# Kernel optimization log

Hardware: AMD Instinct MI355X
Metric: run time of the kernel (lower is better)

Reference implementation:

```python
import jax, jax.numpy as jnp
import numpy as np

B, S, D = 4, 2048, 1024
H = 16
HD = D // H  # 64

def setup_inputs() -> dict:
    key = jax.random.key(0)
    ks = jax.random.split(key, 4)
    scale = 0.02
    return {
        "hidden_states": jax.random.normal(ks[0], (B, S, D), dtype=jnp.float32),
        "attention_mask": jnp.zeros((B, 1, 1, S), dtype=jnp.float32),
        "Wq": jax.random.normal(ks[1], (D, D), dtype=jnp.float32) * scale,
        "bq": jnp.zeros((D,), dtype=jnp.float32),
        "Wk": jax.random.normal(ks[2], (D, D), dtype=jnp.float32) * scale,
        "bk": jnp.zeros((D,), dtype=jnp.float32),
        "Wv": jax.random.normal(ks[3], (D, D), dtype=jnp.float32) * scale,
        "bv": jnp.zeros((D,), dtype=jnp.float32),
    }

def reference(hidden_states, attention_mask, Wq, bq, Wk, bk, Wv, bv):
    b, s, d = hidden_states.shape
    def proj(W, bias):
        # Linear then split heads: [b, s, d] -> [b, H, s, HD]
        y = hidden_states @ W.T + bias
        return y.reshape(b, s, H, HD).transpose(0, 2, 1, 3)
    Q = proj(Wq, bq)
    K = proj(Wk, bk)
    V = proj(Wv, bv)
    scores = jnp.einsum('bhqd,bhkd->bhqk', Q, K) / jnp.sqrt(jnp.float32(HD))
    scores = scores + attention_mask  # additive mask, broadcast [b,1,1,s]
    probs = jax.nn.softmax(scores, axis=-1)
    # dropout prob = 0.0 (eval-mode): identity
    context = jnp.einsum('bhqk,bhkd->bhqd', probs, V)
    return context.transpose(0, 2, 1, 3).reshape(b, s, d)
```

## Files before the change

### kernel.cpp

```cpp
#include <hip/hip_runtime.h>


typedef short bf16x4 __attribute__((ext_vector_type(4)));
typedef short bf16x8 __attribute__((ext_vector_type(8)));
typedef float f32x4 __attribute__((ext_vector_type(4)));

#define SEQ 2048
#define DIM 1024
#define NH 16
#define HDIM 64
#define QKV_ELEMS ((size_t)64 * SEQ * HDIM)

#define WS_FLAG  50331648ull
#define WS_XBF   50331904ull
#define WS_WBF   67109120ull
#define WS_BF32  73400576ull
#define WS_NEED  73412868ull

#define LOG2E 1.4426950408889634f
#define QSCALE (0.125f * LOG2E)

static __device__ __forceinline__ unsigned short f2bf(float f) {
  union { float f; unsigned u; } x; x.f = f;
  unsigned r = x.u + 0x7fffu + ((x.u >> 16) & 1u);
  return (unsigned short)(r >> 16);
}
static __device__ __forceinline__ float bf2f(unsigned short h) {
  union { unsigned u; float f; } x; x.u = ((unsigned)h) << 16;
  return x.f;
}
static __device__ __forceinline__ unsigned pk2bf(float a, float b) {
  union { float f; unsigned u; } x, y; x.f = a; y.f = b;
  return __builtin_amdgcn_perm(y.u + 0x8000u, x.u + 0x8000u, 0x07060302u);
}
static __device__ __forceinline__ int vswz(int s) {
  return (s & ~31) | (((s >> 2) & 3) << 3) | (((s >> 4) & 1) << 2);
}

template <bool FP32>
static __device__ __forceinline__ float load1(const void* p, size_t i) {
  if (FP32) return ((const float*)p)[i];
  else      return bf2f(((const unsigned short*)p)[i]);
}
template <bool FP32>
static __device__ __forceinline__ bf16x8 load8bf(const void* p, size_t i) {
  if (FP32) {
    f32x4 a = *(const f32x4*)((const float*)p + i);
    f32x4 b = *(const f32x4*)((const float*)p + i + 4);
    union { bf16x8 v; unsigned short u[8]; } r;
#pragma unroll
    for (int j = 0; j < 4; ++j) { r.u[j] = f2bf(a[j]); r.u[4 + j] = f2bf(b[j]); }
    return r.v;
  } else {
    return *(const bf16x8*)((const unsigned short*)p + i);
  }
}

static __device__ __forceinline__ void glds16(const unsigned short* g, unsigned short* l) {
  __builtin_amdgcn_global_load_lds(
      (const __attribute__((address_space(1))) unsigned int*)(unsigned long long)(const void*)g,
      (__attribute__((address_space(3))) unsigned int*)(unsigned int)(unsigned long long)(void*)l,
      16, 0, 0);
}

__global__ void detect_dtype(const unsigned short* __restrict__ X, int* __restrict__ flag) {
  __shared__ int zc[256], bc[256];
  int z = 0, b = 0;
  for (int i = threadIdx.x; i < 16384; i += 256) {
    unsigned short u = X[2 * i];
    if (u == 0) z++;
    int e = (u >> 7) & 0xff;
    if (e >= 134) b++;
  }
  zc[threadIdx.x] = z; bc[threadIdx.x] = b;
  __syncthreads();
  for (int s = 128; s > 0; s >>= 1) {
    if (threadIdx.x < s) { zc[threadIdx.x] += zc[threadIdx.x + s]; bc[threadIdx.x] += bc[threadIdx.x + s]; }
    __syncthreads();
  }
  if (threadIdx.x == 0)
    *flag = (zc[0] > 8192 || bc[0] > 64) ? 1 : 0;
}

template <bool FP32>
__global__ void convert_all(const void* __restrict__ X,
                            const void* __restrict__ Wq, const void* __restrict__ Wk,
                            const void* __restrict__ Wv,
                            const void* __restrict__ bq, const void* __restrict__ bk,
                            const void* __restrict__ bv,
                            unsigned char* __restrict__ ws, const int* __restrict__ flag) {
  if (*flag != (FP32 ? 1 : 0)) return;
  unsigned short* Xb = (unsigned short*)(ws + WS_XBF);
  unsigned short* Wb = (unsigned short*)(ws + WS_WBF);
  float* Bb = (float*)(ws + WS_BF32);
  int blk = blockIdx.x;
  if (blk < 4096) {
    size_t base = ((size_t)blk * 256 + threadIdx.x) * 8;
    *(bf16x8*)(Xb + base) = load8bf<FP32>(X, base);
  } else if (blk < 5632) {
    int w = (blk - 4096) >> 9;
    int r = (blk - 4096) & 511;
    const void* W = (w == 0) ? Wq : (w == 1) ? Wk : Wv;
    size_t base = ((size_t)r * 256 + threadIdx.x) * 8;
    *(bf16x8*)(Wb + (size_t)w * 1048576 + base) = load8bf<FP32>(W, base);
  } else {
    int w = blk - 5632;
    const void* Bsrc = (w == 0) ? bq : (w == 1) ? bk : bv;
    for (int i = threadIdx.x; i < 1024; i += 256)
      Bb[w * 1024 + i] = load1<FP32>(Bsrc, i);
  }
}

__global__ __launch_bounds__(256) void qkv_bf(
    const unsigned short* __restrict__ Xb, const unsigned short* __restrict__ Wb,
    const float* __restrict__ Bb,
    unsigned short* __restrict__ Qo, unsigned short* __restrict__ Ko,
    unsigned short* __restrict__ Vo)
{
  const int z = blockIdx.z;
  const unsigned short* W = Wb + (size_t)z * 1048576;

  __shared__ __align__(16) unsigned short Xs[128 * 64];
  __shared__ __align__(16) unsigned short Ws[128 * 64];

  const int tid  = threadIdx.x;
  const int wave = tid >> 6;
  const int lane = tid & 63;
  const int col  = lane & 15;
  const int quad = lane >> 4;
  const int wr = wave & 1;
  const int wc = wave >> 1;
  const int m0 = blockIdx.x * 128;
  const int n0 = blockIdx.y * 128;

  f32x4 zero4 = {0.f, 0.f, 0.f, 0.f};
  f32x4 acc[4][4];
#pragma unroll
  for (int i = 0; i < 4; ++i)
#pragma unroll
    for (int j = 0; j < 4; ++j) acc[i][j] = zero4;

  const int srow8 = lane >> 3;
  const int sseg  = lane & 7;

  for (int k0 = 0; k0 < DIM; k0 += 64) {
    __syncthreads();
#pragma unroll
    for (int a = 0; a < 4; ++a) {
      int rowbase = wave * 32 + a * 8;
      int row = rowbase + srow8;
      int lseg = sseg ^ (row & 7);
      glds16(Xb + (size_t)(m0 + row) * DIM + k0 + lseg * 8, Xs + rowbase * 64);
      glds16(W  + (size_t)(n0 + row) * DIM + k0 + lseg * 8, Ws + rowbase * 64);
    }
    __syncthreads();

#pragma unroll
    for (int kk = 0; kk < 2; ++kk) {
      bf16x8 Af[4], Bf[4];
#pragma unroll
      for (int i = 0; i < 4; ++i) {
        int ra = wr * 64 + i * 16 + col;
        Af[i] = *(const bf16x8*)(Xs + ra * 64 + ((kk * 4 + quad) ^ (ra & 7)) * 8);
        int rb = wc * 64 + i * 16 + col;
        Bf[i] = *(const bf16x8*)(Ws + rb * 64 + ((kk * 4 + quad) ^ (rb & 7)) * 8);
      }
#pragma unroll
      for (int i = 0; i < 4; ++i)
#pragma unroll
        for (int j = 0; j < 4; ++j)
          acc[i][j] = __builtin_amdgcn_mfma_f32_16x16x32_bf16(Af[i], Bf[j], acc[i][j], 0, 0, 0);
    }
  }

  const float oscale = (z == 0) ? QSCALE : 1.0f;
  if (z < 2) {
    unsigned short* Yo = (z == 0) ? Qo : Ko;
#pragma unroll
    for (int i = 0; i < 4; ++i) {
#pragma unroll
      for (int j = 0; j < 4; ++j) {
        int n = n0 + wc * 64 + j * 16 + col;
        float bvf = Bb[z * 1024 + n];
        int h = n >> 6, hd = n & 63;
#pragma unroll
        for (int r = 0; r < 4; ++r) {
          int m = m0 + wr * 64 + i * 16 + quad * 4 + r;
          int b = m >> 11, s = m & 2047;
          Yo[((size_t)(b * NH + h) * SEQ + s) * HDIM + hd] = f2bf((acc[i][j][r] + bvf) * oscale);
        }
      }
    }
  } else {
#pragma unroll
    for (int i = 0; i < 4; ++i) {
#pragma unroll
      for (int j = 0; j < 4; ++j) {
        int n = n0 + wc * 64 + j * 16 + col;
        float bvf = Bb[2 * 1024 + n];
        int h = n >> 6, hd = n & 63;
        int mbase = m0 + wr * 64 + i * 16 + quad * 4;
        int b = mbase >> 11, s = mbase & 2047;
        unsigned long long pk = 0;
#pragma unroll
        for (int r = 0; r < 4; ++r)
          pk |= (unsigned long long)f2bf(acc[i][j][r] + bvf) << (16 * r);
        *(unsigned long long*)(Vo + ((size_t)(b * NH + h) * HDIM + hd) * SEQ + vswz(s)) = pk;
      }
    }
  }
}

#define XS_STRIDE 40
template <bool FP32>
__global__ __launch_bounds__(256) void qkv_any(
    const void* __restrict__ X,
    const void* __restrict__ Wq, const void* __restrict__ bq,
    const void* __restrict__ Wk, const void* __restrict__ bk,
    const void* __restrict__ Wv, const void* __restrict__ bv,
    unsigned short* __restrict__ Qo, unsigned short* __restrict__ Ko,
    unsigned short* __restrict__ Vo, const int* __restrict__ flag)
{
  if (*flag != (FP32 ? 1 : 0)) return;
  const int z = blockIdx.z;
  const void* W    = (z == 0) ? Wq : (z == 1) ? Wk : Wv;
  const void* bias = (z == 0) ? bq : (z == 1) ? bk : bv;

  __shared__ __align__(16) unsigned short Xs[128 * XS_STRIDE];
  __shared__ __align__(16) unsigned short Ws[128 * XS_STRIDE];

  const int tid  = threadIdx.x;
  const int wave = tid >> 6;
  const int lane = tid & 63;
  const int col  = lane & 15;
  const int quad = lane >> 4;
  const int wr = wave & 1;
  const int wc = wave >> 1;
  const int m0 = blockIdx.x * 128;
  const int n0 = blockIdx.y * 128;

  f32x4 zero4 = {0.f, 0.f, 0.f, 0.f};
  f32x4 acc[4][4];
#pragma unroll
  for (int i = 0; i < 4; ++i)
#pragma unroll
    for (int j = 0; j < 4; ++j) acc[i][j] = zero4;

  const int srow = tid >> 2;
  const int sseg = (tid & 3) << 3;

  for (int k0 = 0; k0 < DIM; k0 += 32) {
    __syncthreads();
#pragma unroll
    for (int a = 0; a < 2; ++a) {
      int r = a * 64 + srow;
      *(bf16x8*)(Xs + r * XS_STRIDE + sseg) = load8bf<FP32>(X, (size_t)(m0 + r) * DIM + k0 + sseg);
      *(bf16x8*)(Ws + r * XS_STRIDE + sseg) = load8bf<FP32>(W, (size_t)(n0 + r) * DIM + k0 + sseg);
    }
    __syncthreads();

    bf16x8 Af[4], Bf[4];
#pragma unroll
    for (int i = 0; i < 4; ++i)
      Af[i] = *(const bf16x8*)(Xs + (wr * 64 + i * 16 + col) * XS_STRIDE + quad * 8);
#pragma unroll
    for (int j = 0; j < 4; ++j)
      Bf[j] = *(const bf16x8*)(Ws + (wc * 64 + j * 16 + col) * XS_STRIDE + quad * 8);
#pragma unroll
    for (int i = 0; i < 4; ++i)
#pragma unroll
      for (int j = 0; j < 4; ++j)
        acc[i][j] = __builtin_amdgcn_mfma_f32_16x16x32_bf16(Af[i], Bf[j], acc[i][j], 0, 0, 0);
  }

  const float oscale = (z == 0) ? QSCALE : 1.0f;
  if (z < 2) {
    unsigned short* Yo = (z == 0) ? Qo : Ko;
#pragma unroll
    for (int i = 0; i < 4; ++i) {
#pragma unroll
      for (int j = 0; j < 4; ++j) {
        int n = n0 + wc * 64 + j * 16 + col;
        float bvf = load1<FP32>(bias, n);
        int h = n >> 6, hd = n & 63;
#pragma unroll
        for (int r = 0; r < 4; ++r) {
          int m = m0 + wr * 64 + i * 16 + quad * 4 + r;
          int b = m >> 11, s = m & 2047;
          Yo[((size_t)(b * NH + h) * SEQ + s) * HDIM + hd] = f2bf((acc[i][j][r] + bvf) * oscale);
        }
      }
    }
  } else {
#pragma unroll
    for (int i = 0; i < 4; ++i) {
#pragma unroll
      for (int j = 0; j < 4; ++j) {
        int n = n0 + wc * 64 + j * 16 + col;
        float bvf = load1<FP32>(bias, n);
        int h = n >> 6, hd = n & 63;
        int mbase = m0 + wr * 64 + i * 16 + quad * 4;
        int b = mbase >> 11, s = mbase & 2047;
        unsigned long long pk = 0;
#pragma unroll
        for (int r = 0; r < 4; ++r)
          pk |= (unsigned long long)f2bf(acc[i][j][r] + bvf) << (16 * r);
        *(unsigned long long*)(Vo + ((size_t)(b * NH + h) * HDIM + hd) * SEQ + vswz(s)) = pk;
      }
    }
  }
}

template <bool FP32>
__global__ __launch_bounds__(256, 2) void attn_kernel(
    const unsigned short* __restrict__ Q,
    const unsigned short* __restrict__ K,
    const unsigned short* __restrict__ Vt,
    const void* __restrict__ mask,
    void* __restrict__ OutV, const int* __restrict__ flag)
{
  if (*flag != (FP32 ? 1 : 0)) return;

  __shared__ __align__(16) unsigned short Ks[2 * 128 * 64];
  __shared__ __align__(16) unsigned short Vs[2 * 64 * 128];
  __shared__ __align__(16) float Msall[SEQ];

  const int tid  = threadIdx.x;
  const int wave = tid >> 6;
  const int lane = tid & 63;
  const int col  = lane & 15;
  const int quad = lane >> 4;
  const int qt = blockIdx.x;
  const int bh = blockIdx.y;
  const int b  = bh >> 4;
  const int h  = bh & 15;

  const unsigned short* Qb = Q  + (size_t)bh * SEQ * HDIM;
  const unsigned short* Kb = K  + (size_t)bh * SEQ * HDIM;
  const unsigned short* Vb = Vt + (size_t)bh * HDIM * SEQ;

  if (FP32) {
    const float* mp = (const float*)mask + (size_t)b * SEQ + tid * 8;
    f32x4 a = *(const f32x4*)mp;
    f32x4 c = *(const f32x4*)(mp + 4);
#pragma unroll
    for (int j = 0; j < 4; ++j) {
      Msall[tid * 8 + j]     = a[j] * LOG2E;
      Msall[tid * 8 + 4 + j] = c[j] * LOG2E;
    }
  } else {
    const unsigned short* mp = (const unsigned short*)mask + (size_t)b * SEQ + tid * 8;
    bf16x8 v = *(const bf16x8*)mp;
#pragma unroll
    for (int j = 0; j < 8; ++j)
      Msall[tid * 8 + j] = bf2f((unsigned short)v[j]) * LOG2E;
  }

  const int qrow0 = qt * 128 + wave * 32 + col;
  const int qrow1 = qrow0 + 16;
  const bf16x8 Qf00 = *(const bf16x8*)(Qb + (size_t)qrow0 * HDIM + quad * 8);
  const bf16x8 Qf01 = *(const bf16x8*)(Qb + (size_t)qrow0 * HDIM + 32 + quad * 8);
  const bf16x8 Qf10 = *(const bf16x8*)(Qb + (size_t)qrow1 * HDIM + quad * 8);
  const bf16x8 Qf11 = *(const bf16x8*)(Qb + (size_t)qrow1 * HDIM + 32 + quad * 8);

  const f32x4 z4 = {0.f, 0.f, 0.f, 0.f};
  f32x4 Oacc0[4], Oacc1[4];
  f32x4 Osum0 = z4, Osum1 = z4;
#pragma unroll
  for (int t = 0; t < 4; ++t) { Oacc0[t] = z4; Oacc1[t] = z4; }
  float mrun0 = -1e30f, mrun1 = -1e30f;

  union { bf16x8 v; unsigned u[4]; } ones;
#pragma unroll
  for (int i = 0; i < 4; ++i) ones.u[i] = 0x3F803F80u;

  const int krow_in = lane >> 3;
  const int kphys   = lane & 7;
  const int vrow_in = lane >> 4;
  const int vphys   = lane & 15;

  auto stage = [&](int ktn, int bufn) {
    unsigned short* Kdst = Ks + bufn * (128 * 64);
    unsigned short* Vdst = Vs + bufn * (64 * 128);
#pragma unroll
    for (int a = 0; a < 4; ++a) {
      int row = wave * 32 + a * 8 + krow_in;
      int lseg = kphys ^ (row & 7);
      glds16(Kb + (size_t)(ktn * 128 + row) * HDIM + lseg * 8,
             Kdst + (wave * 32 + a * 8) * 64);
    }
#pragma unroll
    for (int a = 0; a < 4; ++a) {
      int row = wave * 16 + a * 4 + vrow_in;
      int lseg = vphys ^ (row & 15);
      glds16(Vb + (size_t)row * SEQ + ktn * 128 + lseg * 8,
             Vdst + (wave * 16 + a * 4) * 128);
    }
  };

  stage(0, 0);

  for (int kt = 0; kt < 16; ++kt) {
    __syncthreads();
    if (kt < 15) stage(kt + 1, (kt + 1) & 1);

    const unsigned short* Kcur = Ks + (kt & 1) * (128 * 64);
    const unsigned short* Vcur = Vs + (kt & 1) * (64 * 128);
    const float* Mc = Msall + kt * 128;

    f32x4 st0[8], st1[8];
#pragma unroll
    for (int t = 0; t < 8; ++t) {
      const unsigned short* kr = Kcur + (t * 16 + col) * 64;
      bf16x8 Ka = *(const bf16x8*)(kr + (quad ^ (col & 7)) * 8);
      bf16x8 Kc = *(const bf16x8*)(kr + ((4 + quad) ^ (col & 7)) * 8);
      f32x4 c = *(const f32x4*)(Mc + t * 16 + quad * 4);
      f32x4 d0 = c, d1 = c;
      d0 = __builtin_amdgcn_mfma_f32_16x16x32_bf16(Ka, Qf00, d0, 0, 0, 0);
      d0 = __builtin_amdgcn_mfma_f32_16x16x32_bf16(Kc, Qf01, d0, 0, 0, 0);
      d1 = __builtin_amdgcn_mfma_f32_16x16x32_bf16(Ka, Qf10, d1, 0, 0, 0);
      d1 = __builtin_amdgcn_mfma_f32_16x16x32_bf16(Kc, Qf11, d1, 0, 0, 0);
      st0[t] = d0; st1[t] = d1;
    }

    f32x4 m40 = st0[0], m41 = st1[0];
#pragma unroll
    for (int t = 1; t < 8; ++t)
#pragma unroll
      for (int r = 0; r < 4; ++r) {
        m40[r] = fmaxf(m40[r], st0[t][r]);
        m41[r] = fmaxf(m41[r], st1[t][r]);
      }
    float pm0 = fmaxf(fmaxf(m40[0], m40[1]), fmaxf(m40[2], m40[3]));
    float pm1 = fmaxf(fmaxf(m41[0], m41[1]), fmaxf(m41[2], m41[3]));
    pm0 = fmaxf(pm0, __shfl_xor(pm0, 16, 64));
    pm0 = fmaxf(pm0, __shfl_xor(pm0, 32, 64));
    pm1 = fmaxf(pm1, __shfl_xor(pm1, 16, 64));
    pm1 = fmaxf(pm1, __shfl_xor(pm1, 32, 64));

    if (!__all((pm0 - mrun0 <= 8.0f) && (pm1 - mrun1 <= 8.0f))) {
      float mn0 = fmaxf(mrun0, pm0), mn1 = fmaxf(mrun1, pm1);
      float a0 = __builtin_amdgcn_exp2f(mrun0 - mn0);
      float a1 = __builtin_amdgcn_exp2f(mrun1 - mn1);
      mrun0 = mn0; mrun1 = mn1;
      float av0[4], av1[4];
#pragma unroll
      for (int r = 0; r < 4; ++r) {
        av0[r] = __shfl(a0, quad * 4 + r, 64);
        av1[r] = __shfl(a1, quad * 4 + r, 64);
      }
#pragma unroll
      for (int t = 0; t < 4; ++t)
#pragma unroll
        for (int r = 0; r < 4; ++r) {
          Oacc0[t][r] *= av0[r];
          Oacc1[t][r] *= av1[r];
        }
#pragma unroll
      for (int r = 0; r < 4; ++r) { Osum0[r] *= av0[r]; Osum1[r] *= av1[r]; }
    }

#pragma unroll
    for (int t = 0; t < 8; ++t)
#pragma unroll
      for (int r = 0; r < 4; ++r) {
        st0[t][r] = __builtin_amdgcn_exp2f(st0[t][r] - mrun0);
        st1[t][r] = __builtin_amdgcn_exp2f(st1[t][r] - mrun1);
      }

#pragma unroll
    for (int tp = 0; tp < 4; ++tp) {
      union { bf16x8 v; unsigned u[4]; } A0, A1;
      A0.u[0] = pk2bf(st0[2 * tp][0],     st0[2 * tp][1]);
      A0.u[1] = pk2bf(st0[2 * tp][2],     st0[2 * tp][3]);
      A0.u[2] = pk2bf(st0[2 * tp + 1][0], st0[2 * tp + 1][1]);
      A0.u[3] = pk2bf(st0[2 * tp + 1][2], st0[2 * tp + 1][3]);
      A1.u[0] = pk2bf(st1[2 * tp][0],     st1[2 * tp][1]);
      A1.u[1] = pk2bf(st1[2 * tp][2],     st1[2 * tp][3]);
      A1.u[2] = pk2bf(st1[2 * tp + 1][0], st1[2 * tp + 1][1]);
      A1.u[3] = pk2bf(st1[2 * tp + 1][2], st1[2 * tp + 1][3]);
      Osum0 = __builtin_amdgcn_mfma_f32_16x16x32_bf16(A0.v, ones.v, Osum0, 0, 0, 0);
      Osum1 = __builtin_amdgcn_mfma_f32_16x16x32_bf16(A1.v, ones.v, Osum1, 0, 0, 0);
#pragma unroll
      for (int t2 = 0; t2 < 4; ++t2) {
        bf16x8 Bv = *(const bf16x8*)(Vcur + (t2 * 16 + col) * 128 + ((tp * 4 + quad) ^ col) * 8);
        Oacc0[t2] = __builtin_amdgcn_mfma_f32_16x16x32_bf16(A0.v, Bv, Oacc0[t2], 0, 0, 0);
        Oacc1[t2] = __builtin_amdgcn_mfma_f32_16x16x32_bf16(A1.v, Bv, Oacc1[t2], 0, 0, 0);
      }
    }
  }

  float liv0[4], liv1[4];
#pragma unroll
  for (int r = 0; r < 4; ++r) { liv0[r] = 1.0f / Osum0[r]; liv1[r] = 1.0f / Osum1[r]; }
#pragma unroll
  for (int t2 = 0; t2 < 4; ++t2) {
#pragma unroll
    for (int r = 0; r < 4; ++r) {
      int q0 = qt * 128 + wave * 32 + quad * 4 + r;
      int q1 = q0 + 16;
      float v0 = Oacc0[t2][r] * liv0[r];
      float v1 = Oacc1[t2][r] * liv1[r];
      v0 = (v0 == v0) ? v0 : 0.0f;
      v1 = (v1 == v1) ? v1 : 0.0f;
      size_t o0 = ((size_t)b * SEQ + q0) * DIM + h * HDIM + t2 * 16 + col;
      size_t o1 = ((size_t)b * SEQ + q1) * DIM + h * HDIM + t2 * 16 + col;
      if (FP32) {
        ((float*)OutV)[o0] = v0;
        ((float*)OutV)[o1] = v1;
      } else {
        ((unsigned short*)OutV)[o0] = f2bf(v0);
        ((unsigned short*)OutV)[o1] = f2bf(v1);
      }
    }
  }
}

extern "C" void kernel_launch(void* const* d_in, const int* in_sizes, int n_in,
                              void* d_out, int out_size, void* d_ws, size_t ws_size,
                              hipStream_t stream) {
  const void* X    = d_in[0];
  const void* mask = d_in[1];
  const void* Wq   = d_in[2];
  const void* bq   = d_in[3];
  const void* Wk   = d_in[4];
  const void* bk   = d_in[5];
  const void* Wv   = d_in[6];
  const void* bv   = d_in[7];

  unsigned char* ws = (unsigned char*)d_ws;
  unsigned short* Qw = (unsigned short*)ws;
  unsigned short* Kw = Qw + QKV_ELEMS;
  unsigned short* Vw = Kw + QKV_ELEMS;
  int* flag = (int*)(ws + WS_FLAG);

  detect_dtype<<<1, 256, 0, stream>>>((const unsigned short*)X, flag);

  if (ws_size >= WS_NEED) {
    convert_all<false><<<5635, 256, 0, stream>>>(X, Wq, Wk, Wv, bq, bk, bv, ws, flag);
    convert_all<true ><<<5635, 256, 0, stream>>>(X, Wq, Wk, Wv, bq, bk, bv, ws, flag);
    qkv_bf<<<dim3(64, 8, 3), 256, 0, stream>>>(
        (const unsigned short*)(ws + WS_XBF), (const unsigned short*)(ws + WS_WBF),
        (const float*)(ws + WS_BF32), Qw, Kw, Vw);
  } else {
    qkv_any<false><<<dim3(64, 8, 3), 256, 0, stream>>>(X, Wq, bq, Wk, bk, Wv, bv, Qw, Kw, Vw, flag);
    qkv_any<true ><<<dim3(64, 8, 3), 256, 0, stream>>>(X, Wq, bq, Wk, bk, Wv, bv, Qw, Kw, Vw, flag);
  }

  attn_kernel<false><<<dim3(16, 64), 256, 0, stream>>>(Qw, Kw, Vw, mask, d_out, flag);
  attn_kernel<true ><<<dim3(16, 64), 256, 0, stream>>>(Qw, Kw, Vw, mask, d_out, flag);
}
```

Baseline: 269.8 us.

## Use 512-thread attention blocks with 256 query rows, hardware bf16 pack, and MFMA priority

The attention kernel now runs 8 waves per block, each still handling 32 query rows, so one block covers 256 queries. Each K/V tile staged into shared memory is therefore reused by twice as many queries, and each wave issues half as many staging loads. The manual bf16 packing is replaced by the v_cvt_pk_bf16_f32 instruction, and s_setprio brackets the MFMA sections to favour matrix issue across waves. The launch bound of (512,4) tightens register limits and may cause spills. Halving the grid also reduces block-level parallelism.

```diff
diff --git a/kernel.cpp b/kernel.cpp
--- a/kernel.cpp
+++ b/kernel.cpp
@@ -29,9 +29,10 @@
   union { unsigned u; float f; } x; x.u = ((unsigned)h) << 16;
   return x.f;
 }
-static __device__ __forceinline__ unsigned pk2bf(float a, float b) {
-  union { float f; unsigned u; } x, y; x.f = a; y.f = b;
-  return __builtin_amdgcn_perm(y.u + 0x8000u, x.u + 0x8000u, 0x07060302u);
+static __device__ __forceinline__ unsigned cvtpk(float a, float b) {
+  unsigned r;
+  asm("v_cvt_pk_bf16_f32 %0, %1, %2" : "=v"(r) : "v"(a), "v"(b));
+  return r;
 }
 static __device__ __forceinline__ int vswz(int s) {
   return (s & ~31) | (((s >> 2) & 3) << 3) | (((s >> 4) & 1) << 2);
@@ -312,7 +313,7 @@
 }
 
 template <bool FP32>
-__global__ __launch_bounds__(256, 2) void attn_kernel(
+__global__ __launch_bounds__(512, 4) void attn_kernel(
     const unsigned short* __restrict__ Q,
     const unsigned short* __restrict__ K,
     const unsigned short* __restrict__ Vt,
@@ -339,24 +340,22 @@
   const unsigned short* Kb = K  + (size_t)bh * SEQ * HDIM;
   const unsigned short* Vb = Vt + (size_t)bh * HDIM * SEQ;
 
-  if (FP32) {
-    const float* mp = (const float*)mask + (size_t)b * SEQ + tid * 8;
-    f32x4 a = *(const f32x4*)mp;
-    f32x4 c = *(const f32x4*)(mp + 4);
-#pragma unroll
-    for (int j = 0; j < 4; ++j) {
-      Msall[tid * 8 + j]     = a[j] * LOG2E;
-      Msall[tid * 8 + 4 + j] = c[j] * LOG2E;
-    }
-  } else {
-    const unsigned short* mp = (const unsigned short*)mask + (size_t)b * SEQ + tid * 8;
-    bf16x8 v = *(const bf16x8*)mp;
-#pragma unroll
-    for (int j = 0; j < 8; ++j)
-      Msall[tid * 8 + j] = bf2f((unsigned short)v[j]) * LOG2E;
-  }
-
-  const int qrow0 = qt * 128 + wave * 32 + col;
+  {
+    if (FP32) {
+      f32x4 a = *(const f32x4*)((const float*)mask + (size_t)b * SEQ + tid * 4);
+#pragma unroll
+      for (int j = 0; j < 4; ++j) a[j] *= LOG2E;
+      *(f32x4*)(Msall + tid * 4) = a;
+    } else {
+      bf16x4 v = *(const bf16x4*)((const unsigned short*)mask + (size_t)b * SEQ + tid * 4);
+      f32x4 a;
+#pragma unroll
+      for (int j = 0; j < 4; ++j) a[j] = bf2f((unsigned short)v[j]) * LOG2E;
+      *(f32x4*)(Msall + tid * 4) = a;
+    }
+  }
+
+  const int qrow0 = qt * 256 + wave * 32 + col;
   const int qrow1 = qrow0 + 16;
   const bf16x8 Qf00 = *(const bf16x8*)(Qb + (size_t)qrow0 * HDIM + quad * 8);
   const bf16x8 Qf01 = *(const bf16x8*)(Qb + (size_t)qrow0 * HDIM + 32 + quad * 8);
@@ -383,18 +382,18 @@
     unsigned short* Kdst = Ks + bufn * (128 * 64);
     unsigned short* Vdst = Vs + bufn * (64 * 128);
 #pragma unroll
-    for (int a = 0; a < 4; ++a) {
-      int row = wave * 32 + a * 8 + krow_in;
+    for (int a = 0; a < 2; ++a) {
+      int row = wave * 16 + a * 8 + krow_in;
       int lseg = kphys ^ (row & 7);
       glds16(Kb + (size_t)(ktn * 128 + row) * HDIM + lseg * 8,
-             Kdst + (wave * 32 + a * 8) * 64);
-    }
-#pragma unroll
-    for (int a = 0; a < 4; ++a) {
-      int row = wave * 16 + a * 4 + vrow_in;
+             Kdst + (wave * 16 + a * 8) * 64);
+    }
+#pragma unroll
+    for (int a = 0; a < 2; ++a) {
+      int row = wave * 8 + a * 4 + vrow_in;
       int lseg = vphys ^ (row & 15);
       glds16(Vb + (size_t)row * SEQ + ktn * 128 + lseg * 8,
-             Vdst + (wave * 16 + a * 4) * 128);
+             Vdst + (wave * 8 + a * 4) * 128);
     }
   };
 
@@ -409,6 +408,7 @@
     const float* Mc = Msall + kt * 128;
 
     f32x4 st0[8], st1[8];
+    __builtin_amdgcn_s_setprio(1);
 #pragma unroll
     for (int t = 0; t < 8; ++t) {
       const unsigned short* kr = Kcur + (t * 16 + col) * 64;
@@ -422,6 +422,7 @@
       d1 = __builtin_amdgcn_mfma_f32_16x16x32_bf16(Kc, Qf11, d1, 0, 0, 0);
       st0[t] = d0; st1[t] = d1;
     }
+    __builtin_amdgcn_s_setprio(0);
 
     f32x4 m40 = st0[0], m41 = st1[0];
 #pragma unroll
@@ -468,17 +469,18 @@
         st1[t][r] = __builtin_amdgcn_exp2f(st1[t][r] - mrun1);
       }
 
+    __builtin_amdgcn_s_setprio(1);
 #pragma unroll
     for (int tp = 0; tp < 4; ++tp) {
       union { bf16x8 v; unsigned u[4]; } A0, A1;
-      A0.u[0] = pk2bf(st0[2 * tp][0],     st0[2 * tp][1]);
-      A0.u[1] = pk2bf(st0[2 * tp][2],     st0[2 * tp][3]);
-      A0.u[2] = pk2bf(st0[2 * tp + 1][0], st0[2 * tp + 1][1]);
-      A0.u[3] = pk2bf(st0[2 * tp + 1][2], st0[2 * tp + 1][3]);
-      A1.u[0] = pk2bf(st1[2 * tp][0],     st1[2 * tp][1]);
-      A1.u[1] = pk2bf(st1[2 * tp][2],     st1[2 * tp][3]);
-      A1.u[2] = pk2bf(st1[2 * tp + 1][0], st1[2 * tp + 1][1]);
-      A1.u[3] = pk2bf(st1[2 * tp + 1][2], st1[2 * tp + 1][3]);
+      A0.u[0] = cvtpk(st0[2 * tp][0],     st0[2 * tp][1]);
+      A0.u[1] = cvtpk(st0[2 * tp][2],     st0[2 * tp][3]);
+      A0.u[2] = cvtpk(st0[2 * tp + 1][0], st0[2 * tp + 1][1]);
+      A0.u[3] = cvtpk(st0[2 * tp + 1][2], st0[2 * tp + 1][3]);
+      A1.u[0] = cvtpk(st1[2 * tp][0],     st1[2 * tp][1]);
+      A1.u[1] = cvtpk(st1[2 * tp][2],     st1[2 * tp][3]);
+      A1.u[2] = cvtpk(st1[2 * tp + 1][0], st1[2 * tp + 1][1]);
+      A1.u[3] = cvtpk(st1[2 * tp + 1][2], st1[2 * tp + 1][3]);
       Osum0 = __builtin_amdgcn_mfma_f32_16x16x32_bf16(A0.v, ones.v, Osum0, 0, 0, 0);
       Osum1 = __builtin_amdgcn_mfma_f32_16x16x32_bf16(A1.v, ones.v, Osum1, 0, 0, 0);
 #pragma unroll
@@ -488,6 +490,7 @@
         Oacc1[t2] = __builtin_amdgcn_mfma_f32_16x16x32_bf16(A1.v, Bv, Oacc1[t2], 0, 0, 0);
       }
     }
+    __builtin_amdgcn_s_setprio(0);
   }
 
   float liv0[4], liv1[4];
@@ -497,7 +500,7 @@
   for (int t2 = 0; t2 < 4; ++t2) {
 #pragma unroll
     for (int r = 0; r < 4; ++r) {
-      int q0 = qt * 128 + wave * 32 + quad * 4 + r;
+      int q0 = qt * 256 + wave * 32 + quad * 4 + r;
       int q1 = q0 + 16;
       float v0 = Oacc0[t2][r] * liv0[r];
       float v1 = Oacc1[t2][r] * liv1[r];
@@ -547,6 +550,6 @@
     qkv_any<true ><<<dim3(64, 8, 3), 256, 0, stream>>>(X, Wq, bq, Wk, bk, Wv, bv, Qw, Kw, Vw, flag);
   }
 
-  attn_kernel<false><<<dim3(16, 64), 256, 0, stream>>>(Qw, Kw, Vw, mask, d_out, flag);
-  attn_kernel<true ><<<dim3(16, 64), 256, 0, stream>>>(Qw, Kw, Vw, mask, d_out, flag);
-}
+  attn_kernel<false><<<dim3(8, 64), 512, 0, stream>>>(Qw, Kw, Vw, mask, d_out, flag);
+  attn_kernel<true ><<<dim3(8, 64), 512, 0, stream>>>(Qw, Kw, Vw, mask, d_out, flag);
+}
```

Result: slower. 358.0 us (+32.7%).
